# Kernel tuning notes

Measured on AMD Instinct MI355X. Metric: run time of the kernel, lower is better.

Reference implementation:

```python
import jax, jax.numpy as jnp
import numpy as np

LN_EPS = 1e-5


def _gconv(src, dst, x, W, b, n_nodes):
    # DGL GraphConv, norm='both': D_out^{-1/2} A D_in^{-1/2} x W + b
    E = src.shape[0]
    ones = jnp.ones((E,), dtype=x.dtype)
    out_deg = jnp.clip(jax.ops.segment_sum(ones, src, num_segments=n_nodes), 1.0)
    in_deg = jnp.clip(jax.ops.segment_sum(ones, dst, num_segments=n_nodes), 1.0)
    x = x * jax.lax.rsqrt(out_deg)[:, None]
    agg = jax.ops.segment_sum(x[src], dst, num_segments=n_nodes)  # [N, d]
    agg = agg * jax.lax.rsqrt(in_deg)[:, None]
    return agg @ W + b


def _branch(src, dst, x, W1, b1, W2, b2, n_nodes):
    h = jax.nn.relu(_gconv(src, dst, x, W1, b1, n_nodes))  # dropout: eval mode = identity
    return _gconv(src, dst, h, W2, b2, n_nodes)


def _layer_norm(x, g, b):
    mu = jnp.mean(x, axis=-1, keepdims=True)
    var = jnp.mean(jnp.square(x - mu), axis=-1, keepdims=True)
    return (x - mu) * jax.lax.rsqrt(var + LN_EPS) * g + b


def setup_inputs() -> dict:
    key = jax.random.key(0)
    ks = jax.random.split(key, 16)
    N, E, H = 50000, 800000, 128
    Hh = H // 2
    s = lambda fan: 1.0 / np.sqrt(fan)
    u = lambda k, shape, fan: jax.random.uniform(k, shape, jnp.float32, -s(fan), s(fan))
    return {
        "features": jax.random.normal(ks[0], (N, H), jnp.float32),
        "src": jax.random.randint(ks[1], (E,), 0, N),
        "dst": jax.random.randint(ks[2], (E,), 0, N),
        "W1a": u(ks[3], (H, H), H), "b1a": jnp.zeros((H,), jnp.float32),
        "W2a": u(ks[4], (H, Hh), H), "b2a": jnp.zeros((Hh,), jnp.float32),
        "W1b": u(ks[5], (H, H), H), "b1b": jnp.zeros((H,), jnp.float32),
        "W2b": u(ks[6], (H, Hh), H), "b2b": jnp.zeros((Hh,), jnp.float32),
        "Wf1": u(ks[7], (H, H), H), "bf1": u(ks[8], (H,), H),
        "Wf2": u(ks[9], (H, H), H), "bf2": u(ks[10], (H,), H),
        "ln_g": jnp.ones((H,), jnp.float32), "ln_b": jnp.zeros((H,), jnp.float32),
        "n_nodes": N,
    }


def reference(features, src, dst, W1a, b1a, W2a, b2a, W1b, b1b, W2b, b2b,
              Wf1, bf1, Wf2, bf2, ln_g, ln_b, n_nodes):
    ha = _branch(src, dst, features, W1a, b1a, W2a, b2a, n_nodes)  # [N, H/2]
    hb = _branch(src, dst, features, W1b, b1b, W2b, b2b, n_nodes)  # [N, H/2]
    h = jnp.concatenate([ha, hb], axis=-1)  # [N, H]
    h = features + _layer_norm(h, ln_g, ln_b)
    ff = jax.nn.relu(h @ Wf1 + bf1) @ Wf2 + bf2  # dropout eval = identity
    return h + ff
```

## Files before the change

kernel.cpp:

```cpp
#include <hip/hip_runtime.h>

#define LN_EPS 1e-5f
#define NBLK 512
#define BSH  7
#define MAXB 512

typedef __attribute__((ext_vector_type(8))) short bf16x8;
typedef __attribute__((ext_vector_type(4))) float f32x4;

#define MFMA_B16(a, b, c) __builtin_amdgcn_mfma_f32_16x16x32_bf16((a), (b), (c), 0, 0, 0)

__device__ __forceinline__ float bflo(unsigned int u) {
  return __builtin_bit_cast(float, u << 16);
}
__device__ __forceinline__ float bfhi(unsigned int u) {
  return __builtin_bit_cast(float, u & 0xffff0000u);
}
__device__ __forceinline__ float bfs(unsigned short u) {
  return __builtin_bit_cast(float, (unsigned int)u << 16);
}
__device__ __forceinline__ unsigned short f2bf(float f) {
  unsigned int u = __builtin_bit_cast(unsigned int, f);
  u += 0x7fffu + ((u >> 16) & 1u);
  return (unsigned short)(u >> 16);
}
__device__ __forceinline__ float degrs(int d) { return rsqrtf((float)max(d, 1)); }

__global__ __launch_bounds__(256)
void bucket_hist(const int* __restrict__ src, const int* __restrict__ dst,
                 int* __restrict__ blk_cnt, int E, int nbk) {
  __shared__ int h[2 * MAXB];
  int b = blockIdx.x, t = threadIdx.x;
  for (int i = t; i < nbk; i += 256) { h[i] = 0; h[MAXB + i] = 0; }
  __syncthreads();
  int chunk = (E + NBLK - 1) / NBLK;
  int beg = b * chunk, end = min(E, beg + chunk);
  for (int i = beg + t; i < end; i += 256) {
    atomicAdd(&h[dst[i] >> BSH], 1);
    atomicAdd(&h[MAXB + (src[i] >> BSH)], 1);
  }
  __syncthreads();
  for (int i = t; i < nbk; i += 256) {
    blk_cnt[(size_t)i * NBLK + b] = h[i];
    blk_cnt[(size_t)(nbk + i) * NBLK + b] = h[MAXB + i];
  }
}

__global__ __launch_bounds__(256)
void scan_partial_g(const int* __restrict__ v, int* __restrict__ part, int L) {
  __shared__ int sd[256];
  int base = blockIdx.x * 1024;
  int t = threadIdx.x;
  int s = 0;
#pragma unroll
  for (int i = 0; i < 4; ++i) { int idx = base + t * 4 + i; if (idx < L) s += v[idx]; }
  sd[t] = s; __syncthreads();
  for (int o = 128; o > 0; o >>= 1) { if (t < o) sd[t] += sd[t + o]; __syncthreads(); }
  if (t == 0) part[blockIdx.x] = sd[0];
}

__global__ __launch_bounds__(256)
void scan_final_g(const int* __restrict__ v, const int* __restrict__ part,
                  int* __restrict__ off, int L) {
  __shared__ int sd[256];
  __shared__ int pex_s;
  int base = blockIdx.x * 1024;
  int t = threadIdx.x;
  if (t < 64) {
    int p = 0;
    for (int i = t; i < (int)blockIdx.x; i += 64) p += part[i];
#pragma unroll
    for (int o = 1; o < 64; o <<= 1) p += __shfl_xor(p, o, 64);
    if (t == 0) pex_s = p;
  }
  int loc[4]; int s = 0;
#pragma unroll
  for (int i = 0; i < 4; ++i) {
    int idx = base + t * 4 + i;
    loc[i] = (idx < L) ? v[idx] : 0;
    s += loc[i];
  }
  sd[t] = s; __syncthreads();
  for (int o = 1; o < 256; o <<= 1) {
    int x = (t >= o) ? sd[t - o] : 0;
    __syncthreads();
    sd[t] += x;
    __syncthreads();
  }
  int excl = sd[t] - s + pex_s;
#pragma unroll
  for (int i = 0; i < 4; ++i) {
    int idx = base + t * 4 + i;
    if (idx < L) off[idx] = excl;
    excl += loc[i];
  }
}

__global__ __launch_bounds__(256)
void bucket_scatter(const int* __restrict__ src, const int* __restrict__ dst,
                    const int* __restrict__ off, unsigned int* __restrict__ pairs,
                    int E, int nbk) {
  __shared__ int cur[2 * MAXB];
  int b = blockIdx.x, t = threadIdx.x;
  for (int i = t; i < nbk; i += 256) {
    cur[i] = off[(size_t)i * NBLK + b];
    cur[MAXB + i] = off[(size_t)(nbk + i) * NBLK + b];
  }
  __syncthreads();
  int chunk = (E + NBLK - 1) / NBLK;
  int beg = b * chunk, end = min(E, beg + chunk);
  for (int i = beg + t; i < end; i += 256) {
    int d = dst[i], s = src[i];
    int p1 = atomicAdd(&cur[d >> BSH], 1);
    pairs[p1] = ((unsigned int)s << BSH) | (unsigned int)(d & 127);
    int p2 = atomicAdd(&cur[MAXB + (s >> BSH)], 1);
    pairs[p2] = (unsigned int)(s & 127);
  }
}

__global__ __launch_bounds__(256)
void bucket_finish(const unsigned int* __restrict__ pairs, const int* __restrict__ off,
                   int* __restrict__ row_off, int* __restrict__ deg_d,
                   int* __restrict__ deg_s, int* __restrict__ csr_src,
                   int N, int E, int nbk) {
  __shared__ int h[128];
  __shared__ int cur[128];
  int g = blockIdx.x, t = threadIdx.x;
  if (t < 128) h[t] = 0;
  __syncthreads();
  if (g < nbk) {
    int base = off[(size_t)g * NBLK];
    int end  = off[(size_t)(g + 1) * NBLK];
    for (int i = base + t; i < end; i += 256) atomicAdd(&h[pairs[i] & 127], 1);
    __syncthreads();
    int orig = (t < 128) ? h[t] : 0;
    for (int o = 1; o < 128; o <<= 1) {
      int v = (t < 128 && t >= o) ? h[t - o] : 0;
      __syncthreads();
      if (t < 128) h[t] += v;
      __syncthreads();
    }
    if (t < 128) {
      int excl = base + h[t] - orig;
      cur[t] = excl;
      int node = (g << BSH) + t;
      if (node < N) { row_off[node] = excl; deg_d[node] = orig; }
    }
    if (g == nbk - 1 && t == 0) row_off[N] = E;
    __syncthreads();
    for (int i = base + t; i < end; i += 256) {
      unsigned int v = pairs[i];
      int pos = atomicAdd(&cur[v & 127], 1);
      csr_src[pos] = (int)(v >> BSH);
    }
  } else {
    int j = g - nbk;
    int beg = off[(size_t)(nbk + j) * NBLK];
    int end = (j + 1 < nbk) ? off[(size_t)(nbk + j + 1) * NBLK] : 2 * E;
    for (int i = beg + t; i < end; i += 256) atomicAdd(&h[pairs[i] & 127], 1);
    __syncthreads();
    int nb0 = j << BSH;
    if (t < 128 && nb0 + t < N) deg_s[nb0 + t] = h[t];
  }
}

__global__ __launch_bounds__(256)
void convert_all(const float* __restrict__ x, const int* __restrict__ deg_s,
                 unsigned short* __restrict__ xb, int n4,
                 const float* __restrict__ W1a, const float* __restrict__ W1b,
                 const float* __restrict__ W2a, const float* __restrict__ W2b,
                 const float* __restrict__ Wf1, const float* __restrict__ Wf2,
                 unsigned short* __restrict__ w1aT, unsigned short* __restrict__ w1bT,
                 unsigned short* __restrict__ w2aT, unsigned short* __restrict__ w2bT,
                 unsigned short* __restrict__ wf1T, unsigned short* __restrict__ wf2T) {
  const int featB = (n4 + 255) >> 8;
  int b = blockIdx.x, t = threadIdx.x;
  if (b < featB) {
    int i = b * 256 + t;
    if (i < n4) {
      float sc = degrs(deg_s[i >> 5]);
      float4 v = reinterpret_cast<const float4*>(x)[i];
      ushort4 r;
      r.x = f2bf(v.x * sc); r.y = f2bf(v.y * sc); r.z = f2bf(v.z * sc); r.w = f2bf(v.w * sc);
      reinterpret_cast<ushort4*>(xb)[i] = r;
    }
  } else {
    const float* S; unsigned short* D; int NC;
    switch (b - featB) {
      case 0: S = W1a; D = w1aT; NC = 128; break;
      case 1: S = W1b; D = w1bT; NC = 128; break;
      case 2: S = W2a; D = w2aT; NC = 64;  break;
      case 3: S = W2b; D = w2bT; NC = 64;  break;
      case 4: S = Wf1; D = wf1T; NC = 128; break;
      default: S = Wf2; D = wf2T; NC = 128; break;
    }
    int total = 128 * NC;
    for (int i = t; i < total; i += 256) {
      int k = i / NC, n = i - k * NC;
      D[n * 128 + k] = f2bf(S[i]);
    }
  }
}

__global__ __launch_bounds__(256)
void gather128b(const int* __restrict__ row_off, const int* __restrict__ csr_src,
                const unsigned short* __restrict__ xb,
                unsigned short* __restrict__ ob, int N) {
  int n = blockIdx.x * 4 + (threadIdx.x >> 6);
  if (n >= N) return;
  int lane = threadIdx.x & 63;
  int ch = lane & 15, es = lane >> 4;
  int beg = row_off[n], end = row_off[n + 1];
  float a[8] = {0.f, 0.f, 0.f, 0.f, 0.f, 0.f, 0.f, 0.f};
  int k = beg + es;
  for (; k + 4 < end; k += 8) {
    int s0 = csr_src[k], s1 = csr_src[k + 4];
    uint4 v0 = *reinterpret_cast<const uint4*>(xb + (size_t)s0 * 128 + ch * 8);
    uint4 v1 = *reinterpret_cast<const uint4*>(xb + (size_t)s1 * 128 + ch * 8);
    a[0] += bflo(v0.x) + bflo(v1.x); a[1] += bfhi(v0.x) + bfhi(v1.x);
    a[2] += bflo(v0.y) + bflo(v1.y); a[3] += bfhi(v0.y) + bfhi(v1.y);
    a[4] += bflo(v0.z) + bflo(v1.z); a[5] += bfhi(v0.z) + bfhi(v1.z);
    a[6] += bflo(v0.w) + bflo(v1.w); a[7] += bfhi(v0.w) + bfhi(v1.w);
  }
  if (k < end) {
    int s0 = csr_src[k];
    uint4 v0 = *reinterpret_cast<const uint4*>(xb + (size_t)s0 * 128 + ch * 8);
    a[0] += bflo(v0.x); a[1] += bfhi(v0.x);
    a[2] += bflo(v0.y); a[3] += bfhi(v0.y);
    a[4] += bflo(v0.z); a[5] += bfhi(v0.z);
    a[6] += bflo(v0.w); a[7] += bfhi(v0.w);
  }
#pragma unroll
  for (int o = 16; o < 64; o <<= 1)
#pragma unroll
    for (int i = 0; i < 8; ++i) a[i] += __shfl_xor(a[i], o, 64);
  if (es == 0) {
    uint4 r;
    r.x = (unsigned int)f2bf(a[0]) | ((unsigned int)f2bf(a[1]) << 16);
    r.y = (unsigned int)f2bf(a[2]) | ((unsigned int)f2bf(a[3]) << 16);
    r.z = (unsigned int)f2bf(a[4]) | ((unsigned int)f2bf(a[5]) << 16);
    r.w = (unsigned int)f2bf(a[6]) | ((unsigned int)f2bf(a[7]) << 16);
    *reinterpret_cast<uint4*>(ob + (size_t)n * 128 + ch * 8) = r;
  }
}

__global__ __launch_bounds__(256)
void gemm_mid_lds(const unsigned short* __restrict__ aggb,
                  const unsigned short* __restrict__ w1aT, const float* __restrict__ b1a,
                  const unsigned short* __restrict__ w1bT, const float* __restrict__ b1b,
                  const unsigned short* __restrict__ w2aT,
                  const unsigned short* __restrict__ w2bT,
                  const int* __restrict__ deg_s, const int* __restrict__ deg_d,
                  unsigned short* __restrict__ zb, int N) {
  __shared__ unsigned short w1s[128 * 128];
  __shared__ unsigned short h1s[64 * 128];
  int br = blockIdx.y;
  const unsigned short* w1T = br ? w1bT : w1aT;
  const float* b1 = br ? b1b : b1a;
  const unsigned short* w2T = br ? w2bT : w2aT;
  int t = threadIdx.x, wid = t >> 6, lane = t & 63;
  int m0 = blockIdx.x * 64;
  int ll = lane & 15, lg = lane >> 4;
  int rA = wid * 16 + ll;
  int rw0 = m0 + wid * 16 + lg * 4;
  int rl0 = wid * 16 + lg * 4;

  const unsigned short* ap = aggb + (size_t)min(m0 + rA, N - 1) * 128 + lg * 8;
  bf16x8 A[4];
#pragma unroll
  for (int k = 0; k < 4; ++k) A[k] = *reinterpret_cast<const bf16x8*>(ap + k * 32);

  float rsi[4], rso[4];
#pragma unroll
  for (int j = 0; j < 4; ++j) {
    int m = min(rw0 + j, N - 1);
    rsi[j] = degrs(deg_d[m]);
    rso[j] = degrs(deg_s[m]);
  }

  {
    char* w1c = (char*)w1s;
#pragma unroll
    for (int it = 0; it < 8; ++it) {
      int i = t + it * 256;
      int row = i >> 4;
      int cb = (i & 15) << 4;
      uint4 v = *reinterpret_cast<const uint4*>(w1T + row * 128 + (cb >> 1));
      *reinterpret_cast<uint4*>(w1c + row * 256 + (cb ^ ((row & 7) << 4))) = v;
    }
  }
  __syncthreads();

  const char* w1c = (const char*)w1s;
#pragma unroll
  for (int c = 0; c < 8; ++c) {
    int row = c * 16 + ll;
    int swb = (row & 7) << 4;
    f32x4 acc = {0.f, 0.f, 0.f, 0.f};
#pragma unroll
    for (int k = 0; k < 4; ++k) {
      bf16x8 B = *reinterpret_cast<const bf16x8*>(w1c + row * 256 + ((lg * 16 + k * 64) ^ swb));
      acc = MFMA_B16(A[k], B, acc);
    }
    int n = c * 16 + ll;
    float bv = b1[n];
#pragma unroll
    for (int j = 0; j < 4; ++j) {
      float v = fmaxf(fmaf(acc[j], rsi[j], bv), 0.f) * rso[j];
      int r = rl0 + j;
      h1s[r * 128 + (n ^ ((r & 7) << 3))] = f2bf(v);
    }
  }

  bf16x8 A2[4];
#pragma unroll
  for (int k = 0; k < 4; ++k)
    A2[k] = *reinterpret_cast<const bf16x8*>(
        h1s + rA * 128 + ((lg * 8 + k * 32) ^ ((rA & 7) << 3)));
#pragma unroll
  for (int c = 0; c < 4; ++c) {
    const unsigned short* bp = w2T + (size_t)(c * 16 + ll) * 128 + lg * 8;
    f32x4 acc = {0.f, 0.f, 0.f, 0.f};
#pragma unroll
    for (int k = 0; k < 4; ++k)
      acc = MFMA_B16(A2[k], *reinterpret_cast<const bf16x8*>(bp + k * 32), acc);
    int n = br * 64 + c * 16 + ll;
#pragma unroll
    for (int j = 0; j < 4; ++j) {
      int m = rw0 + j;
      if (m < N) zb[(size_t)m * 128 + n] = f2bf(acc[j]);
    }
  }
}

__global__ __launch_bounds__(256)
void fused_tail5(const unsigned short* __restrict__ agg2z,
                 const unsigned short* __restrict__ featb,
                 const float* __restrict__ b2a, const float* __restrict__ b2b,
                 const int* __restrict__ deg_s, const int* __restrict__ deg_d,
                 const float* __restrict__ ln_g, const float* __restrict__ ln_b,
                 const unsigned short* __restrict__ wf1T, const float* __restrict__ bf1,
                 const unsigned short* __restrict__ wf2T, const float* __restrict__ bf2,
                 float* __restrict__ out, int N) {
  __shared__ unsigned short wf1s[128 * 128];
  __shared__ unsigned short wf2s[128 * 128];
  __shared__ unsigned short hsb[64 * 128];
  unsigned short* ffb = wf1s;
  int t = threadIdx.x, wid = t >> 6, lane = t & 63;
  int m0 = blockIdx.x * 64;
  int ll = lane & 15, lg = lane >> 4;
  int rl0 = wid * 16 + lg * 4;

  {
    char* d1 = (char*)wf1s;
    char* d2 = (char*)wf2s;
#pragma unroll
    for (int it = 0; it < 8; ++it) {
      int i = t + it * 256;
      int row = i >> 4;
      int cb = (i & 15) << 4;
      uint4 v1 = *reinterpret_cast<const uint4*>(wf1T + row * 128 + (cb >> 1));
      uint4 v2 = *reinterpret_cast<const uint4*>(wf2T + row * 128 + (cb >> 1));
      *reinterpret_cast<uint4*>(d1 + row * 256 + (cb ^ ((row & 7) << 4))) = v1;
      *reinterpret_cast<uint4*>(d2 + row * 256 + (cb ^ ((row & 7) << 4))) = v2;
    }
  }

  float rsv[4], sqs[4];
#pragma unroll
  for (int j = 0; j < 4; ++j) {
    int m = min(m0 + rl0 + j, N - 1);
    rsv[j] = degrs(deg_d[m]);
    sqs[j] = sqrtf((float)max(deg_s[m], 1));
  }

  float x[8][4];
  float s[4] = {0.f, 0.f, 0.f, 0.f}, q[4] = {0.f, 0.f, 0.f, 0.f};
#pragma unroll
  for (int ct = 0; ct < 8; ++ct) {
    int n = ct * 16 + ll;
    float bv = (n < 64) ? b2a[n] : b2b[n - 64];
#pragma unroll
    for (int j = 0; j < 4; ++j) {
      int m = min(m0 + rl0 + j, N - 1);
      float v = fmaf(bfs(agg2z[(size_t)m * 128 + n]), rsv[j], bv);
      x[ct][j] = v;
      s[j] += v;
      q[j] += v * v;
    }
  }

#pragma unroll
  for (int o = 1; o < 16; o <<= 1) {
#pragma unroll
    for (int j = 0; j < 4; ++j) {
      s[j] += __shfl_xor(s[j], o, 64);
      q[j] += __shfl_xor(q[j], o, 64);
    }
  }
  float mu[4], rstd[4];
#pragma unroll
  for (int j = 0; j < 4; ++j) {
    mu[j] = s[j] * (1.f / 128.f);
    float var = fmaxf(q[j] * (1.f / 128.f) - mu[j] * mu[j], 0.f);
    rstd[j] = rsqrtf(var + LN_EPS);
  }
#pragma unroll
  for (int ct = 0; ct < 8; ++ct) {
    int n = ct * 16 + ll;
    float gv = ln_g[n], bv = ln_b[n];
#pragma unroll
    for (int j = 0; j < 4; ++j) {
      int m = min(m0 + rl0 + j, N - 1);
      float fv = bfs(featb[(size_t)m * 128 + n]) * sqs[j];
      float hv = fv + (x[ct][j] - mu[j]) * rstd[j] * gv + bv;
      x[ct][j] = hv;
      int r = rl0 + j;
      hsb[r * 128 + (n ^ ((r & 7) << 3))] = f2bf(hv);
    }
  }
  __syncthreads();

  float xf[8][4];
  {
    int rloc = wid * 16 + ll;
    int swr = (rloc & 7) << 3;
    bf16x8 A[4];
#pragma unroll
    for (int k = 0; k < 4; ++k)
      A[k] = *reinterpret_cast<const bf16x8*>(hsb + rloc * 128 + ((lg * 8 + k * 32) ^ swr));
    const char* w1c = (const char*)wf1s;
#pragma unroll
    for (int c = 0; c < 8; ++c) {
      int row = c * 16 + ll;
      int swb = (row & 7) << 4;
      f32x4 a = {0.f, 0.f, 0.f, 0.f};
#pragma unroll
      for (int k = 0; k < 4; ++k) {
        bf16x8 B = *reinterpret_cast<const bf16x8*>(w1c + row * 256 + ((lg * 16 + k * 64) ^ swb));
        a = MFMA_B16(A[k], B, a);
      }
      float bv = bf1[c * 16 + ll];
#pragma unroll
      for (int j = 0; j < 4; ++j) xf[c][j] = fmaxf(a[j] + bv, 0.f);
    }
  }
  __syncthreads();

#pragma unroll
  for (int c = 0; c < 8; ++c) {
    int n = c * 16 + ll;
#pragma unroll
    for (int j = 0; j < 4; ++j) {
      int r = rl0 + j;
      ffb[r * 128 + (n ^ ((r & 7) << 3))] = f2bf(xf[c][j]);
    }
  }

  {
    int rloc = wid * 16 + ll;
    int swr = (rloc & 7) << 3;
    bf16x8 A[4];
#pragma unroll
    for (int k = 0; k < 4; ++k)
      A[k] = *reinterpret_cast<const bf16x8*>(ffb + rloc * 128 + ((lg * 8 + k * 32) ^ swr));
    const char* w2c = (const char*)wf2s;
#pragma unroll
    for (int c = 0; c < 8; ++c) {
      int row = c * 16 + ll;
      int swb = (row & 7) << 4;
      f32x4 a = {0.f, 0.f, 0.f, 0.f};
#pragma unroll
      for (int k = 0; k < 4; ++k) {
        bf16x8 B = *reinterpret_cast<const bf16x8*>(w2c + row * 256 + ((lg * 16 + k * 64) ^ swb));
        a = MFMA_B16(A[k], B, a);
      }
      int n = c * 16 + ll;
      float bv = bf2[n];
#pragma unroll
      for (int j = 0; j < 4; ++j) {
        int m = m0 + rl0 + j;
        if (m < N) out[(size_t)m * 128 + n] = x[c][j] + a[j] + bv;
      }
    }
  }
}

extern "C" void kernel_launch(void* const* d_in, const int* in_sizes, int n_in,
                              void* d_out, int out_size, void* d_ws, size_t ws_size,
                              hipStream_t stream) {
  const float* features = (const float*)d_in[0];
  const int*   src      = (const int*)d_in[1];
  const int*   dst      = (const int*)d_in[2];
  const float* W1a = (const float*)d_in[3];  const float* b1a = (const float*)d_in[4];
  const float* W2a = (const float*)d_in[5];  const float* b2a = (const float*)d_in[6];
  const float* W1b = (const float*)d_in[7];  const float* b1b = (const float*)d_in[8];
  const float* W2b = (const float*)d_in[9];  const float* b2b = (const float*)d_in[10];
  const float* Wf1 = (const float*)d_in[11]; const float* bf1 = (const float*)d_in[12];
  const float* Wf2 = (const float*)d_in[13]; const float* bf2 = (const float*)d_in[14];
  const float* ln_g = (const float*)d_in[15];
  const float* ln_b = (const float*)d_in[16];

  const int N = in_sizes[0] / 128;
  const int E = in_sizes[1];
  float* out = (float*)d_out;

  const int nbk = (N + 127) >> BSH;
  const int L = 2 * nbk * NBLK;

  size_t off_b = 0;
  char* wsb = (char*)d_ws;
  auto take = [&](size_t bytes) -> void* {
    void* p = wsb + off_b;
    off_b += (bytes + 255) & ~(size_t)255;
    return p;
  };
  int* blk_cnt = (int*)take((size_t)L * 4);
  int* boff    = (int*)take((size_t)L * 4);
  int* part    = (int*)take((size_t)1024 * 4);
  unsigned int* pairs = (unsigned int*)take((size_t)2 * E * 4);
  int* deg_s   = (int*)take((size_t)N * 4);
  int* deg_d   = (int*)take((size_t)N * 4);
  int* row_off = (int*)take((size_t)(N + 1) * 4);
  int* csr_src = (int*)take((size_t)E * 4);
  unsigned short* featb = (unsigned short*)take((size_t)N * 128 * 2);
  unsigned short* aggb  = (unsigned short*)take((size_t)N * 128 * 2);
  unsigned short* zb    = (unsigned short*)take((size_t)N * 128 * 2);
  unsigned short* agg2z = (unsigned short*)take((size_t)N * 128 * 2);
  unsigned short* w1aT  = (unsigned short*)take(128 * 128 * 2);
  unsigned short* w1bT  = (unsigned short*)take(128 * 128 * 2);
  unsigned short* w2aT  = (unsigned short*)take(64 * 128 * 2);
  unsigned short* w2bT  = (unsigned short*)take(64 * 128 * 2);
  unsigned short* wf1T  = (unsigned short*)take(128 * 128 * 2);
  unsigned short* wf2T  = (unsigned short*)take(128 * 128 * 2);

  const int gatherBlocks = (N + 3) / 4;
  const int mtiles = (N + 63) / 64;
  const int n4 = (N * 128) / 4;
  const int featB = (n4 + 255) / 256;
  const int scanL = (L + 1023) / 1024;

  bucket_hist<<<NBLK, 256, 0, stream>>>(src, dst, blk_cnt, E, nbk);
  scan_partial_g<<<scanL, 256, 0, stream>>>(blk_cnt, part, L);
  scan_final_g<<<scanL, 256, 0, stream>>>(blk_cnt, part, boff, L);
  bucket_scatter<<<NBLK, 256, 0, stream>>>(src, dst, boff, pairs, E, nbk);
  bucket_finish<<<2 * nbk, 256, 0, stream>>>(
      pairs, boff, row_off, deg_d, deg_s, csr_src, N, E, nbk);
  convert_all<<<featB + 6, 256, 0, stream>>>(
      features, deg_s, featb, n4,
      W1a, W1b, W2a, W2b, Wf1, Wf2,
      w1aT, w1bT, w2aT, w2bT, wf1T, wf2T);
  gather128b<<<gatherBlocks, 256, 0, stream>>>(row_off, csr_src, featb, aggb, N);
  gemm_mid_lds<<<dim3(mtiles, 2), 256, 0, stream>>>(aggb, w1aT, b1a, w1bT, b1b,
                                                    w2aT, w2bT, deg_s, deg_d, zb, N);
  gather128b<<<gatherBlocks, 256, 0, stream>>>(row_off, csr_src, zb, agg2z, N);
  fused_tail5<<<mtiles, 256, 0, stream>>>(agg2z, featb, b2a, b2b,
                                          deg_s, deg_d, ln_g, ln_b,
                                          wf1T, bf1, wf2T, bf2, out, N);
}
```

Measured before the change: 179.7 us.

## Split bf16 node features into four column slices for cache-local gathers

Stores the bf16 feature, aggregate and hidden buffers as four 32-column slices, each holding all nodes contiguously, instead of one row-major 128-column layout. The gather kernel now runs four times as many blocks, each summing one slice with 4 lanes per row and 16 edges in parallel. The goal is to shrink the working set of each gather pass to a quarter so the random neighbour reads hit in L2/MALL more often. In exchange, every node's CSR list is read four times, the per-node reductions need more shuffles, and the GEMM and tail kernels now do strided slice loads and stores.

```diff
diff --git a/kernel.cpp b/kernel.cpp
--- a/kernel.cpp
+++ b/kernel.cpp
@@ -25,6 +25,7 @@
   return (unsigned short)(u >> 16);
 }
 __device__ __forceinline__ float degrs(int d) { return rsqrtf((float)max(d, 1)); }
+
 
 __global__ __launch_bounds__(256)
 void bucket_hist(const int* __restrict__ src, const int* __restrict__ dst,
@@ -166,7 +167,7 @@
 
 __global__ __launch_bounds__(256)
 void convert_all(const float* __restrict__ x, const int* __restrict__ deg_s,
-                 unsigned short* __restrict__ xb, int n4,
+                 unsigned short* __restrict__ xb, int n4, size_t SL,
                  const float* __restrict__ W1a, const float* __restrict__ W1b,
                  const float* __restrict__ W2a, const float* __restrict__ W2b,
                  const float* __restrict__ Wf1, const float* __restrict__ Wf2,
@@ -178,11 +179,12 @@
   if (b < featB) {
     int i = b * 256 + t;
     if (i < n4) {
-      float sc = degrs(deg_s[i >> 5]);
+      int node = i >> 5, c = i & 31;
+      float sc = degrs(deg_s[node]);
       float4 v = reinterpret_cast<const float4*>(x)[i];
       ushort4 r;
       r.x = f2bf(v.x * sc); r.y = f2bf(v.y * sc); r.z = f2bf(v.z * sc); r.w = f2bf(v.w * sc);
-      reinterpret_cast<ushort4*>(xb)[i] = r;
+      *reinterpret_cast<ushort4*>(xb + (size_t)(c >> 3) * SL + (size_t)node * 32 + (c & 7) * 4) = r;
     }
   } else {
     const float* S; unsigned short* D; int NC;
@@ -203,20 +205,24 @@
 }
 
 __global__ __launch_bounds__(256)
-void gather128b(const int* __restrict__ row_off, const int* __restrict__ csr_src,
-                const unsigned short* __restrict__ xb,
-                unsigned short* __restrict__ ob, int N) {
-  int n = blockIdx.x * 4 + (threadIdx.x >> 6);
+void gather32s(const int* __restrict__ row_off, const int* __restrict__ csr_src,
+               const unsigned short* __restrict__ xb,
+               unsigned short* __restrict__ ob, int N, int nodeBlocks, size_t SL) {
+  int bid = blockIdx.x;
+  int slice = bid / nodeBlocks;
+  int nb = bid - slice * nodeBlocks;
+  int n = nb * 4 + (threadIdx.x >> 6);
   if (n >= N) return;
   int lane = threadIdx.x & 63;
-  int ch = lane & 15, es = lane >> 4;
+  int ch = lane & 3, es = lane >> 2;
+  const unsigned short* base = xb + (size_t)slice * SL;
   int beg = row_off[n], end = row_off[n + 1];
   float a[8] = {0.f, 0.f, 0.f, 0.f, 0.f, 0.f, 0.f, 0.f};
   int k = beg + es;
-  for (; k + 4 < end; k += 8) {
-    int s0 = csr_src[k], s1 = csr_src[k + 4];
-    uint4 v0 = *reinterpret_cast<const uint4*>(xb + (size_t)s0 * 128 + ch * 8);
-    uint4 v1 = *reinterpret_cast<const uint4*>(xb + (size_t)s1 * 128 + ch * 8);
+  for (; k + 16 < end; k += 32) {
+    int s0 = csr_src[k], s1 = csr_src[k + 16];
+    uint4 v0 = *reinterpret_cast<const uint4*>(base + (size_t)s0 * 32 + ch * 8);
+    uint4 v1 = *reinterpret_cast<const uint4*>(base + (size_t)s1 * 32 + ch * 8);
     a[0] += bflo(v0.x) + bflo(v1.x); a[1] += bfhi(v0.x) + bfhi(v1.x);
     a[2] += bflo(v0.y) + bflo(v1.y); a[3] += bfhi(v0.y) + bfhi(v1.y);
     a[4] += bflo(v0.z) + bflo(v1.z); a[5] += bfhi(v0.z) + bfhi(v1.z);
@@ -224,28 +230,28 @@
   }
   if (k < end) {
     int s0 = csr_src[k];
-    uint4 v0 = *reinterpret_cast<const uint4*>(xb + (size_t)s0 * 128 + ch * 8);
+    uint4 v0 = *reinterpret_cast<const uint4*>(base + (size_t)s0 * 32 + ch * 8);
     a[0] += bflo(v0.x); a[1] += bfhi(v0.x);
     a[2] += bflo(v0.y); a[3] += bfhi(v0.y);
     a[4] += bflo(v0.z); a[5] += bfhi(v0.z);
     a[6] += bflo(v0.w); a[7] += bfhi(v0.w);
   }
 #pragma unroll
-  for (int o = 16; o < 64; o <<= 1)
+  for (int o = 4; o < 64; o <<= 1)
 #pragma unroll
     for (int i = 0; i < 8; ++i) a[i] += __shfl_xor(a[i], o, 64);
-  if (es == 0) {
+  if (lane < 4) {
     uint4 r;
     r.x = (unsigned int)f2bf(a[0]) | ((unsigned int)f2bf(a[1]) << 16);
     r.y = (unsigned int)f2bf(a[2]) | ((unsigned int)f2bf(a[3]) << 16);
     r.z = (unsigned int)f2bf(a[4]) | ((unsigned int)f2bf(a[5]) << 16);
     r.w = (unsigned int)f2bf(a[6]) | ((unsigned int)f2bf(a[7]) << 16);
-    *reinterpret_cast<uint4*>(ob + (size_t)n * 128 + ch * 8) = r;
-  }
-}
-
-__global__ __launch_bounds__(256)
-void gemm_mid_lds(const unsigned short* __restrict__ aggb,
+    *reinterpret_cast<uint4*>(ob + (size_t)slice * SL + (size_t)n * 32 + lane * 8) = r;
+  }
+}
+
+__global__ __launch_bounds__(256)
+void gemm_mid_lds(const unsigned short* __restrict__ aggb, size_t SL,
                   const unsigned short* __restrict__ w1aT, const float* __restrict__ b1a,
                   const unsigned short* __restrict__ w1bT, const float* __restrict__ b1b,
                   const unsigned short* __restrict__ w2aT,
@@ -265,10 +271,11 @@
   int rw0 = m0 + wid * 16 + lg * 4;
   int rl0 = wid * 16 + lg * 4;
 
-  const unsigned short* ap = aggb + (size_t)min(m0 + rA, N - 1) * 128 + lg * 8;
+  int rowA = min(m0 + rA, N - 1);
   bf16x8 A[4];
 #pragma unroll
-  for (int k = 0; k < 4; ++k) A[k] = *reinterpret_cast<const bf16x8*>(ap + k * 32);
+  for (int k = 0; k < 4; ++k)
+    A[k] = *reinterpret_cast<const bf16x8*>(aggb + (size_t)k * SL + (size_t)rowA * 32 + lg * 8);
 
   float rsi[4], rso[4];
 #pragma unroll
@@ -325,10 +332,11 @@
     for (int k = 0; k < 4; ++k)
       acc = MFMA_B16(A2[k], *reinterpret_cast<const bf16x8*>(bp + k * 32), acc);
     int n = br * 64 + c * 16 + ll;
+    size_t zoff = (size_t)(n >> 5) * SL + (n & 31);
 #pragma unroll
     for (int j = 0; j < 4; ++j) {
       int m = rw0 + j;
-      if (m < N) zb[(size_t)m * 128 + n] = f2bf(acc[j]);
+      if (m < N) zb[zoff + (size_t)m * 32] = f2bf(acc[j]);
     }
   }
 }
@@ -336,6 +344,7 @@
 __global__ __launch_bounds__(256)
 void fused_tail5(const unsigned short* __restrict__ agg2z,
                  const unsigned short* __restrict__ featb,
+                 size_t SL,
                  const float* __restrict__ b2a, const float* __restrict__ b2b,
                  const int* __restrict__ deg_s, const int* __restrict__ deg_d,
                  const float* __restrict__ ln_g, const float* __restrict__ ln_b,
@@ -379,11 +388,12 @@
 #pragma unroll
   for (int ct = 0; ct < 8; ++ct) {
     int n = ct * 16 + ll;
+    size_t noff = (size_t)(n >> 5) * SL + (n & 31);
     float bv = (n < 64) ? b2a[n] : b2b[n - 64];
 #pragma unroll
     for (int j = 0; j < 4; ++j) {
       int m = min(m0 + rl0 + j, N - 1);
-      float v = fmaf(bfs(agg2z[(size_t)m * 128 + n]), rsv[j], bv);
+      float v = fmaf(bfs(agg2z[noff + (size_t)m * 32]), rsv[j], bv);
       x[ct][j] = v;
       s[j] += v;
       q[j] += v * v;
@@ -408,11 +418,12 @@
 #pragma unroll
   for (int ct = 0; ct < 8; ++ct) {
     int n = ct * 16 + ll;
+    size_t noff = (size_t)(n >> 5) * SL + (n & 31);
     float gv = ln_g[n], bv = ln_b[n];
 #pragma unroll
     for (int j = 0; j < 4; ++j) {
       int m = min(m0 + rl0 + j, N - 1);
-      float fv = bfs(featb[(size_t)m * 128 + n]) * sqs[j];
+      float fv = bfs(featb[noff + (size_t)m * 32]) * sqs[j];
       float hv = fv + (x[ct][j] - mu[j]) * rstd[j] * gv + bv;
       x[ct][j] = hv;
       int r = rl0 + j;
@@ -507,6 +518,7 @@
 
   const int nbk = (N + 127) >> BSH;
   const int L = 2 * nbk * NBLK;
+  const size_t SL = (size_t)N * 32;
 
   size_t off_b = 0;
   char* wsb = (char*)d_ws;
@@ -534,7 +546,7 @@
   unsigned short* wf1T  = (unsigned short*)take(128 * 128 * 2);
   unsigned short* wf2T  = (unsigned short*)take(128 * 128 * 2);
 
-  const int gatherBlocks = (N + 3) / 4;
+  const int nodeBlocks = (N + 3) / 4;
   const int mtiles = (N + 63) / 64;
   const int n4 = (N * 128) / 4;
   const int featB = (n4 + 255) / 256;
@@ -547,14 +559,16 @@
   bucket_finish<<<2 * nbk, 256, 0, stream>>>(
       pairs, boff, row_off, deg_d, deg_s, csr_src, N, E, nbk);
   convert_all<<<featB + 6, 256, 0, stream>>>(
-      features, deg_s, featb, n4,
+      features, deg_s, featb, n4, SL,
       W1a, W1b, W2a, W2b, Wf1, Wf2,
       w1aT, w1bT, w2aT, w2bT, wf1T, wf2T);
-  gather128b<<<gatherBlocks, 256, 0, stream>>>(row_off, csr_src, featb, aggb, N);
-  gemm_mid_lds<<<dim3(mtiles, 2), 256, 0, stream>>>(aggb, w1aT, b1a, w1bT, b1b,
+  gather32s<<<4 * nodeBlocks, 256, 0, stream>>>(row_off, csr_src, featb, aggb,
+                                                N, nodeBlocks, SL);
+  gemm_mid_lds<<<dim3(mtiles, 2), 256, 0, stream>>>(aggb, SL, w1aT, b1a, w1bT, b1b,
                                                     w2aT, w2bT, deg_s, deg_d, zb, N);
-  gather128b<<<gatherBlocks, 256, 0, stream>>>(row_off, csr_src, zb, agg2z, N);
-  fused_tail5<<<mtiles, 256, 0, stream>>>(agg2z, featb, b2a, b2b,
+  gather32s<<<4 * nodeBlocks, 256, 0, stream>>>(row_off, csr_src, zb, agg2z,
+                                                N, nodeBlocks, SL);
+  fused_tail5<<<mtiles, 256, 0, stream>>>(agg2z, featb, SL, b2a, b2b,
                                           deg_s, deg_d, ln_g, ln_b,
                                           wf1T, bf1, wf2T, bf2, out, N);
 }
```

After: 256.8 us. 1.43x slower.
